# Kernel tuning notes

Measured on AMD Instinct MI355X. Metric: run time of the kernel, lower is better.

Reference implementation:

```python
import jax, jax.numpy as jnp
import numpy as np

B, LQ, LK, DK, DV = 32, 128, 4096, 256, 256


def setup_inputs() -> dict:
    key = jax.random.key(0)
    k1, k2, k3, k4, k5 = jax.random.split(key, 5)
    return {
        "query": jax.random.normal(k1, (B, LQ, DK), dtype=jnp.float32),
        "query_lengths": jax.random.randint(k2, (B,), 1, LQ, dtype=jnp.int32),
        "keys": jax.random.normal(k3, (B, LK, DK), dtype=jnp.float32),
        "values": jax.random.normal(k4, (B, LK, DV), dtype=jnp.float32),
        "mask": jax.random.randint(k5, (B, LK), 0, 2, dtype=jnp.int32),  # 1 = masked out
    }


def reference(query, query_lengths, keys, values, mask):
    # zero query positions beyond each example's length (torch: mask_query masked_fill 0)
    q_valid = jnp.arange(query.shape[1])[None, :] < query_lengths[:, None]  # [B, Lq]
    query = jnp.where(q_valid[:, :, None], query, 0.0)
    # zero masked key/value timesteps (torch mask: 1 -> masked)
    kv_valid = (mask == 0)[:, :, None]  # [B, Lk, 1]
    keys = jnp.where(kv_valid, keys, 0.0)
    values = jnp.where(kv_valid, values, 0.0)
    # attention scores [B, Lq, Lk]
    weights = jnp.einsum("bqd,bkd->bqk", query, keys)
    # exact-zero scores (masked rows/cols) -> -inf, matching torch weights==0.0 fill
    weights = jnp.where(weights == 0.0, -jnp.inf, weights)
    weights = jax.nn.softmax(weights, axis=-1)
    # rows that were all -inf produce NaN -> cleaned to 0
    weights = jnp.where(jnp.isnan(weights), 0.0, weights)
    attended = jnp.einsum("bqk,bkv->bqv", weights, values)  # [B, Lq, Dv]
    return jnp.mean(attended, axis=1)  # [B, Dv]
```

## Files before the change

### kernel.cpp

```cpp
#include <hip/hip_runtime.h>
#include <hip/hip_fp16.h>
#include <stdint.h>

#define NB  32
#define NLQ 128
#define NLK 4096
#define NDK 256
#define NDV 256
#define KT  16
#define SPLITS 8
#define MINSPLITS 4

typedef _Float16 f16;
typedef _Float16 f16x4 __attribute__((ext_vector_type(4)));
typedef _Float16 f16x8 __attribute__((ext_vector_type(8)));
typedef float    f32x4 __attribute__((ext_vector_type(4)));

__global__ __launch_bounds__(512) void fvta_part1(
    const float* __restrict__ q_, const float* __restrict__ k_,
    const float* __restrict__ v_, const int* __restrict__ mask_,
    f16* __restrict__ accw, float* __restrict__ mlw)
{
    __shared__ __align__(16) f16 KA[2][KT * NDK];
    __shared__ __align__(16) f16 VA[2][KT * NDV];
    __shared__ __align__(16) f16 QA[64 * NDK];
    __shared__ int MK[NLK / MINSPLITS];

    const int tid = threadIdx.x, w = tid >> 6, lane = tid & 63;
    const int l15 = lane & 15, lhi = lane >> 4;
    const int qsub = w >> 1;
    const int dvh  = w & 1;
    const int x = blockIdx.x, b = blockIdx.y;
    const int S = gridDim.x >> 1;
    const int s  = (S == 8) ? (x & 7) : (x >> 1);
    const int qz = (S == 8) ? (x >> 3) : (x & 1);
    const int slice = NLK / S, nt = slice / KT, kbase = s * slice;
    const float NEG = -__builtin_inff();

    const float* kb = k_ + ((size_t)b * NLK + kbase) * NDK;
    const float* vb = v_ + ((size_t)b * NLK + kbase) * NDV;
    const int*   mb = mask_ + b * NLK + kbase;

    for (int i = tid; i < slice; i += 512) MK[i] = mb[i];

    {
        const float* qsrc = q_ + ((size_t)b * NLQ + qz * 64) * NDK;
        #pragma unroll
        for (int r = 0; r < 8; ++r) {
            const int idx = r * 512 + tid;
            const int qq  = idx >> 6;
            const int d   = (idx & 63) * 4;
            f32x4 xv = *(const f32x4*)(qsrc + qq * NDK + d);
            f16x4 hh; hh[0]=(f16)xv[0]; hh[1]=(f16)xv[1]; hh[2]=(f16)xv[2]; hh[3]=(f16)xv[3];
            *(f16x4*)(QA + qq * NDK + (d ^ ((qq & 15) << 3))) = hh;
        }
    }

    f32x4 accu[8];
    #pragma unroll
    for (int i = 0; i < 8; ++i) accu[i] = (f32x4){0.f, 0.f, 0.f, 0.f};
    float m_run = NEG, l_run = 0.f;

    f32x4 ks[2], vs[2];

    auto stage = [&](f16* KAb, f16* VAb) {
        #pragma unroll
        for (int r = 0; r < 2; ++r) {
            const int idx = r * 512 + tid;
            const int kk  = idx >> 6;
            const int d   = (idx & 63) * 4;
            const int e   = kk * NDK + (d ^ (kk << 3));
            f32x4 xv = ks[r];
            f16x4 hh; hh[0]=(f16)xv[0]; hh[1]=(f16)xv[1]; hh[2]=(f16)xv[2]; hh[3]=(f16)xv[3];
            *(f16x4*)(KAb + e) = hh;
            f32x4 yv = vs[r];
            f16x4 gg; gg[0]=(f16)yv[0]; gg[1]=(f16)yv[1]; gg[2]=(f16)yv[2]; gg[3]=(f16)yv[3];
            *(f16x4*)(VAb + e) = gg;
        }
    };

    #pragma unroll
    for (int r = 0; r < 2; ++r) {
        ks[r] = *(const f32x4*)(kb + (r * 512 + tid) * 4);
        vs[r] = *(const f32x4*)(vb + (r * 512 + tid) * 4);
    }
    stage(KA[0], VA[0]);
    __syncthreads();

    const int swz = l15 << 3;

    for (int t = 0; t < nt; ++t) {
        const int cur = t & 1;
        if (t + 1 < nt) {
            const float* ksrc = kb + (size_t)(t + 1) * KT * NDK;
            const float* vsrc = vb + (size_t)(t + 1) * KT * NDV;
            #pragma unroll
            for (int r = 0; r < 2; ++r) {
                ks[r] = *(const f32x4*)(ksrc + (r * 512 + tid) * 4);
                vs[r] = *(const f32x4*)(vsrc + (r * 512 + tid) * 4);
            }
        }
        const int k0 = t * KT;

        f32x4 s4 = (f32x4){0.f,0.f,0.f,0.f};
        {
            const f16* kp = &KA[cur][l15 * NDK];
            const f16* qp = &QA[(qsub * 16 + l15) * NDK];
            #pragma unroll
            for (int kd = 0; kd < 8; ++kd) {
                const int col = (kd * 32 + lhi * 8) ^ swz;
                f16x8 kf = *(const f16x8*)(kp + col);
                f16x8 qv = *(const f16x8*)(qp + col);
                s4 = __builtin_amdgcn_mfma_f32_16x16x32_f16(kf, qv, s4, 0, 0, 0);
            }
        }

        const int4 m4 = *(const int4*)(MK + k0 + lhi * 4);
        float sa[4];
        sa[0] = m4.x ? NEG : s4[0]; sa[1] = m4.y ? NEG : s4[1];
        sa[2] = m4.z ? NEG : s4[2]; sa[3] = m4.w ? NEG : s4[3];

        float tmax = fmaxf(fmaxf(sa[0], sa[1]), fmaxf(sa[2], sa[3]));
        tmax = fmaxf(tmax, __shfl_xor(tmax, 16, 64));
        tmax = fmaxf(tmax, __shfl_xor(tmax, 32, 64));
        const float mnew = fmaxf(m_run, tmax);
        const bool  dead = (mnew == NEG);
        const float scale = dead ? 1.f : __expf(m_run - mnew);
        float p4[4];
        #pragma unroll
        for (int j = 0; j < 4; ++j) p4[j] = dead ? 0.f : __expf(sa[j] - mnew);
        float ps = (p4[0] + p4[1]) + (p4[2] + p4[3]);
        ps += __shfl_xor(ps, 16, 64);
        ps += __shfl_xor(ps, 32, 64);
        l_run = l_run * scale + ps;
        m_run = mnew;

        f16x4 pa;
        pa[0]=(f16)p4[0]; pa[1]=(f16)p4[1]; pa[2]=(f16)p4[2]; pa[3]=(f16)p4[3];

        if (!__all(scale == 1.f)) {
            float scj[4];
            #pragma unroll
            for (int j = 0; j < 4; ++j) scj[j] = __shfl(scale, lhi * 4 + j, 64);
            #pragma unroll
            for (int d = 0; d < 8; ++d) {
                accu[d][0] *= scj[0]; accu[d][1] *= scj[1];
                accu[d][2] *= scj[2]; accu[d][3] *= scj[3];
            }
        }

        {
            const f16* VL = &VA[cur][0];
            #pragma unroll
            for (int dg = 0; dg < 2; ++dg) {
                #pragma unroll
                for (int dd = 0; dd < 4; ++dd) {
                    f16x4 vf;
                    #pragma unroll
                    for (int j = 0; j < 4; ++j) {
                        const int rr  = lhi * 4 + j;
                        const int col = (dvh * 128 + (dg * 4 + dd) * 16 + l15)
                                        ^ (rr << 3);
                        vf[j] = VL[rr * NDV + col];
                    }
                    accu[dg * 4 + dd] = __builtin_amdgcn_mfma_f32_16x16x16f16(
                        pa, vf, accu[dg * 4 + dd], 0, 0, 0);
                }
            }
        }

        if (t + 1 < nt) stage(KA[cur ^ 1], VA[cur ^ 1]);
        __syncthreads();
    }

    const size_t base = (size_t)(b * S + s) * NLQ + qz * 64 + qsub * 16;
    #pragma unroll
    for (int j = 0; j < 4; ++j) {
        f16* dst = accw + (base + lhi * 4 + j) * NDV + dvh * 128 + l15;
        #pragma unroll
        for (int d = 0; d < 8; ++d) dst[d * 16] = (f16)accu[d][j];
    }
    if (dvh == 0 && lane < 16) {
        mlw[(base + lane) * 2]     = m_run;
        mlw[(base + lane) * 2 + 1] = l_run;
    }
}

__global__ __launch_bounds__(256) void fvta_merge(
    const f16* __restrict__ accw, const float* __restrict__ mlw,
    const int* __restrict__ qlen_, float* __restrict__ out_, int S)
{
    __shared__ float fac[8][SPLITS + 1];
    const int qc = blockIdx.x, b = blockIdx.y, tid = threadIdx.x;
    const int len = qlen_[b];
    const float NEG = -__builtin_inff();

    if (tid < 8) {
        const int q = qc * 8 + tid;
        if (q < len) {
            float gm = NEG;
            for (int ss = 0; ss < S; ++ss)
                gm = fmaxf(gm, mlw[((size_t)(b * S + ss) * NLQ + q) * 2]);
            float L = 0.f;
            for (int ss = 0; ss < S; ++ss) {
                const float m = mlw[((size_t)(b * S + ss) * NLQ + q) * 2];
                const float l = mlw[((size_t)(b * S + ss) * NLQ + q) * 2 + 1];
                if (m != NEG) L += l * __expf(m - gm);
            }
            for (int ss = 0; ss < S; ++ss) {
                const float m = mlw[((size_t)(b * S + ss) * NLQ + q) * 2];
                fac[tid][ss] = (gm != NEG && L > 0.f && m != NEG)
                             ? __expf(m - gm) / L : 0.f;
            }
        } else {
            for (int ss = 0; ss < S; ++ss) fac[tid][ss] = 0.f;
        }
    }
    __syncthreads();

    float sum = 0.f;
    for (int qq = 0; qq < 8; ++qq) {
        const int q = qc * 8 + qq;
        for (int ss = 0; ss < S; ++ss) {
            const float f = fac[qq][ss];
            if (f != 0.f)
                sum += (float)accw[((size_t)(b * S + ss) * NLQ + q) * NDV + tid] * f;
        }
    }
    atomicAdd(&out_[b * NDV + tid], sum * (1.f / NLQ));
}

extern "C" void kernel_launch(void* const* d_in, const int* in_sizes, int n_in,
                              void* d_out, int out_size, void* d_ws, size_t ws_size,
                              hipStream_t stream) {
    const float* q    = (const float*)d_in[0];
    const int*   qlen = (const int*)d_in[1];
    const float* k    = (const float*)d_in[2];
    const float* v    = (const float*)d_in[3];
    const int*   mask = (const int*)d_in[4];
    float* out = (float*)d_out;

    int S = SPLITS;
    while (S > MINSPLITS &&
           ((size_t)NB * S * NLQ * NDV * 2 + (size_t)NB * S * NLQ * 8) > ws_size)
        S >>= 1;
    f16*   accw = (f16*)d_ws;
    float* mlw  = (float*)((char*)d_ws + (size_t)NB * S * NLQ * NDV * 2);

    hipMemsetAsync(out, 0, (size_t)out_size * sizeof(float), stream);
    dim3 g1(2 * S, NB);
    fvta_part1<<<g1, 512, 0, stream>>>(q, k, v, mask, accw, mlw);
    dim3 g2(NLQ / 8, NB);
    fvta_merge<<<g2, 256, 0, stream>>>(accw, mlw, qlen, out, S);
}
```

Before: 128.3 us.

## Transpose V in LDS, defer softmax rescale, normalize partials, double the splits

Values are now stored transposed in shared memory with a padded row stride, so each lane fetches its MFMA B-operand with two 32-bit reads instead of four scattered 16-bit reads. The online softmax skips the running-max update and accumulator rescale while every tile's max stays within 8 of the current max. Each split's partial sum is normalized by its own l before being written in fp16, and the merge kernel applies the l-weighted factor. SPLITS goes from 8 to 16 for more parallelism, at the cost of more partial writes and merge work and more transposed-store LDS bank conflicts.

```diff
diff --git a/kernel.cpp b/kernel.cpp
--- a/kernel.cpp
+++ b/kernel.cpp
@@ -8,10 +8,12 @@
 #define NDK 256
 #define NDV 256
 #define KT  16
-#define SPLITS 8
-#define MINSPLITS 4
+#define SPLITS 16
+#define MINSPLITS 8
+#define VST 18
 
 typedef _Float16 f16;
+typedef _Float16 f16x2 __attribute__((ext_vector_type(2)));
 typedef _Float16 f16x4 __attribute__((ext_vector_type(4)));
 typedef _Float16 f16x8 __attribute__((ext_vector_type(8)));
 typedef float    f32x4 __attribute__((ext_vector_type(4)));
@@ -21,9 +23,9 @@
     const float* __restrict__ v_, const int* __restrict__ mask_,
     f16* __restrict__ accw, float* __restrict__ mlw)
 {
+    __shared__ __align__(16) f16 QA[64 * NDK];
     __shared__ __align__(16) f16 KA[2][KT * NDK];
-    __shared__ __align__(16) f16 VA[2][KT * NDV];
-    __shared__ __align__(16) f16 QA[64 * NDK];
+    __shared__ __align__(16) f16 VT[2][NDV * VST];
     __shared__ int MK[NLK / MINSPLITS];
 
     const int tid = threadIdx.x, w = tid >> 6, lane = tid & 63;
@@ -32,8 +34,7 @@
     const int dvh  = w & 1;
     const int x = blockIdx.x, b = blockIdx.y;
     const int S = gridDim.x >> 1;
-    const int s  = (S == 8) ? (x & 7) : (x >> 1);
-    const int qz = (S == 8) ? (x >> 3) : (x & 1);
+    const int s = x >> 1, qz = x & 1;
     const int slice = NLK / S, nt = slice / KT, kbase = s * slice;
     const float NEG = -__builtin_inff();
 
@@ -63,43 +64,39 @@
 
     f32x4 ks[2], vs[2];
 
-    auto stage = [&](f16* KAb, f16* VAb) {
+    auto stage = [&](f16* KAb, f16* VTb) {
         #pragma unroll
         for (int r = 0; r < 2; ++r) {
-            const int idx = r * 512 + tid;
-            const int kk  = idx >> 6;
-            const int d   = (idx & 63) * 4;
-            const int e   = kk * NDK + (d ^ (kk << 3));
+            const int kk = ((r * 512 + tid) >> 6);
+            const int c  = (tid & 63) * 4;
             f32x4 xv = ks[r];
             f16x4 hh; hh[0]=(f16)xv[0]; hh[1]=(f16)xv[1]; hh[2]=(f16)xv[2]; hh[3]=(f16)xv[3];
-            *(f16x4*)(KAb + e) = hh;
+            *(f16x4*)(KAb + kk * NDK + (c ^ (kk << 3))) = hh;
             f32x4 yv = vs[r];
-            f16x4 gg; gg[0]=(f16)yv[0]; gg[1]=(f16)yv[1]; gg[2]=(f16)yv[2]; gg[3]=(f16)yv[3];
-            *(f16x4*)(VAb + e) = gg;
+            #pragma unroll
+            for (int i = 0; i < 4; ++i)
+                VTb[(c + i) * VST + kk] = (f16)yv[i];
         }
     };
-
-    #pragma unroll
-    for (int r = 0; r < 2; ++r) {
-        ks[r] = *(const f32x4*)(kb + (r * 512 + tid) * 4);
-        vs[r] = *(const f32x4*)(vb + (r * 512 + tid) * 4);
-    }
-    stage(KA[0], VA[0]);
+    auto loadKV = [&](int t) {
+        const float* ksrc = kb + (size_t)t * KT * NDK;
+        const float* vsrc = vb + (size_t)t * KT * NDV;
+        #pragma unroll
+        for (int r = 0; r < 2; ++r) {
+            ks[r] = *(const f32x4*)(ksrc + (r * 512 + tid) * 4);
+            vs[r] = *(const f32x4*)(vsrc + (r * 512 + tid) * 4);
+        }
+    };
+
+    loadKV(0);
+    stage(KA[0], VT[0]);
     __syncthreads();
 
     const int swz = l15 << 3;
 
     for (int t = 0; t < nt; ++t) {
         const int cur = t & 1;
-        if (t + 1 < nt) {
-            const float* ksrc = kb + (size_t)(t + 1) * KT * NDK;
-            const float* vsrc = vb + (size_t)(t + 1) * KT * NDV;
-            #pragma unroll
-            for (int r = 0; r < 2; ++r) {
-                ks[r] = *(const f32x4*)(ksrc + (r * 512 + tid) * 4);
-                vs[r] = *(const f32x4*)(vsrc + (r * 512 + tid) * 4);
-            }
-        }
+        if (t + 1 < nt) loadKV(t + 1);
         const int k0 = t * KT;
 
         f32x4 s4 = (f32x4){0.f,0.f,0.f,0.f};
@@ -123,62 +120,70 @@
         float tmax = fmaxf(fmaxf(sa[0], sa[1]), fmaxf(sa[2], sa[3]));
         tmax = fmaxf(tmax, __shfl_xor(tmax, 16, 64));
         tmax = fmaxf(tmax, __shfl_xor(tmax, 32, 64));
-        const float mnew = fmaxf(m_run, tmax);
-        const bool  dead = (mnew == NEG);
-        const float scale = dead ? 1.f : __expf(m_run - mnew);
+
+        const bool defer = (m_run != NEG) && __all(tmax - m_run <= 8.f);
+        if (!defer) {
+            const float mnew = fmaxf(m_run, tmax);
+            if (mnew != NEG) {
+                const float scale = (m_run == NEG) ? 0.f : __expf(m_run - mnew);
+                float scj[4];
+                #pragma unroll
+                for (int j = 0; j < 4; ++j) scj[j] = __shfl(scale, lhi * 4 + j, 64);
+                #pragma unroll
+                for (int d = 0; d < 8; ++d) {
+                    accu[d][0] *= scj[0]; accu[d][1] *= scj[1];
+                    accu[d][2] *= scj[2]; accu[d][3] *= scj[3];
+                }
+                l_run *= scale;
+                m_run = mnew;
+            }
+        }
+
         float p4[4];
-        #pragma unroll
-        for (int j = 0; j < 4; ++j) p4[j] = dead ? 0.f : __expf(sa[j] - mnew);
+        if (m_run == NEG) {
+            #pragma unroll
+            for (int j = 0; j < 4; ++j) p4[j] = 0.f;
+        } else {
+            #pragma unroll
+            for (int j = 0; j < 4; ++j) p4[j] = __expf(sa[j] - m_run);
+        }
         float ps = (p4[0] + p4[1]) + (p4[2] + p4[3]);
         ps += __shfl_xor(ps, 16, 64);
         ps += __shfl_xor(ps, 32, 64);
-        l_run = l_run * scale + ps;
-        m_run = mnew;
+        l_run += ps;
 
         f16x4 pa;
         pa[0]=(f16)p4[0]; pa[1]=(f16)p4[1]; pa[2]=(f16)p4[2]; pa[3]=(f16)p4[3];
 
-        if (!__all(scale == 1.f)) {
-            float scj[4];
-            #pragma unroll
-            for (int j = 0; j < 4; ++j) scj[j] = __shfl(scale, lhi * 4 + j, 64);
+        {
+            const f16* VTc = &VT[cur][0];
             #pragma unroll
             for (int d = 0; d < 8; ++d) {
-                accu[d][0] *= scj[0]; accu[d][1] *= scj[1];
-                accu[d][2] *= scj[2]; accu[d][3] *= scj[3];
-            }
-        }
-
-        {
-            const f16* VL = &VA[cur][0];
-            #pragma unroll
-            for (int dg = 0; dg < 2; ++dg) {
-                #pragma unroll
-                for (int dd = 0; dd < 4; ++dd) {
-                    f16x4 vf;
-                    #pragma unroll
-                    for (int j = 0; j < 4; ++j) {
-                        const int rr  = lhi * 4 + j;
-                        const int col = (dvh * 128 + (dg * 4 + dd) * 16 + l15)
-                                        ^ (rr << 3);
-                        vf[j] = VL[rr * NDV + col];
-                    }
-                    accu[dg * 4 + dd] = __builtin_amdgcn_mfma_f32_16x16x16f16(
-                        pa, vf, accu[dg * 4 + dd], 0, 0, 0);
-                }
-            }
-        }
-
-        if (t + 1 < nt) stage(KA[cur ^ 1], VA[cur ^ 1]);
+                const int dv = dvh * 128 + d * 16 + l15;
+                const f16* vp = VTc + dv * VST + 4 * lhi;
+                f16x2 v0 = *(const f16x2*)(vp);
+                f16x2 v1 = *(const f16x2*)(vp + 2);
+                f16x4 vf; vf[0]=v0[0]; vf[1]=v0[1]; vf[2]=v1[0]; vf[3]=v1[1];
+                accu[d] = __builtin_amdgcn_mfma_f32_16x16x16f16(
+                    pa, vf, accu[d], 0, 0, 0);
+            }
+        }
+
+        if (t + 1 < nt) stage(KA[cur ^ 1], VT[cur ^ 1]);
         __syncthreads();
     }
+
+    const float rl = (l_run > 0.f) ? 1.f / l_run : 0.f;
+    float rlj[4];
+    #pragma unroll
+    for (int j = 0; j < 4; ++j) rlj[j] = __shfl(rl, lhi * 4 + j, 64);
 
     const size_t base = (size_t)(b * S + s) * NLQ + qz * 64 + qsub * 16;
     #pragma unroll
     for (int j = 0; j < 4; ++j) {
         f16* dst = accw + (base + lhi * 4 + j) * NDV + dvh * 128 + l15;
         #pragma unroll
-        for (int d = 0; d < 8; ++d) dst[d * 16] = (f16)accu[d][j];
+        for (int d = 0; d < 8; ++d) dst[d * 16] = (f16)(accu[d][j] * rlj[j]);
     }
     if (dvh == 0 && lane < 16) {
         mlw[(base + lane) * 2]     = m_run;
@@ -209,8 +214,9 @@
             }
             for (int ss = 0; ss < S; ++ss) {
                 const float m = mlw[((size_t)(b * S + ss) * NLQ + q) * 2];
+                const float l = mlw[((size_t)(b * S + ss) * NLQ + q) * 2 + 1];
                 fac[tid][ss] = (gm != NEG && L > 0.f && m != NEG)
-                             ? __expf(m - gm) / L : 0.f;
+                             ? l * __expf(m - gm) / L : 0.f;
             }
         } else {
             for (int ss = 0; ss < S; ++ss) fac[tid][ss] = 0.f;
```

New measurement: 146.9 us. 1.14x slower.
